# Kernel optimization log

Hardware: AMD Instinct MI355X
Metric: run time of the kernel (lower is better)

## Reference

```python
import jax, jax.numpy as jnp
import numpy as np

T = 0.12  # softmax temperature


def _mlp(x, Wa, ba, Wb, bb, Wc, bc):
    # Linear -> ReLU -> (Dropout=id in eval) -> Linear -> ReLU -> Linear -> ReLU
    h = jax.nn.relu(x @ Wa + ba)
    h = jax.nn.relu(h @ Wb + bb)
    return jax.nn.relu(h @ Wc + bc)


def setup_inputs() -> dict:
    key = jax.random.key(0)
    ks = jax.random.split(key, 16)
    B, K, A, P = 2048, 64, 312, 128
    std = 0.01  # torch init: normal(0, 0.01), bias 0
    inp = {
        "v2s": jax.random.normal(ks[0], (B, A), jnp.float32),
        "tar_atts": jax.random.uniform(ks[1], (B, 1), jnp.float32),
        "sample_indices": jax.random.randint(ks[2], (B, K), 0, B),
        # CLproject[1]: 1 -> 1024 -> 2048 -> 312
        "W2a": std * jax.random.normal(ks[3], (1, 1024), jnp.float32),
        "b2a": jnp.zeros((1024,), jnp.float32),
        "W2b": std * jax.random.normal(ks[4], (1024, 2048), jnp.float32),
        "b2b": jnp.zeros((2048,), jnp.float32),
        "W2c": std * jax.random.normal(ks[5], (2048, A), jnp.float32),
        "b2c": jnp.zeros((A,), jnp.float32),
        # CLproject[0]: 312 -> 1024 -> 2048 -> 128
        "W1a": std * jax.random.normal(ks[6], (A, 1024), jnp.float32),
        "b1a": jnp.zeros((1024,), jnp.float32),
        "W1b": std * jax.random.normal(ks[7], (1024, 2048), jnp.float32),
        "b1b": jnp.zeros((2048,), jnp.float32),
        "W1c": std * jax.random.normal(ks[8], (2048, P), jnp.float32),
        "b1c": jnp.zeros((P,), jnp.float32),
    }
    return inp


def reference(v2s, tar_atts, sample_indices, W2a, b2a, W2b, b2b, W2c, b2c,
              W1a, b1a, W1b, b1b, W1c, b1c):
    # attribute embedding via CLproject[1]: [B,1] -> [B,312]
    att = _mlp(tar_atts, W2a, b2a, W2b, b2b, W2c, b2c)
    v2s_sg = jax.lax.stop_gradient(v2s)  # detach().clone()
    # gather padded pos+neg sample lists: [B,K,312]
    samples = v2s_sg[sample_indices]
    # per-sample projection via CLproject[0]
    proj_samples = _mlp(samples + att[:, None, :], W1a, b1a, W1b, b1b, W1c, b1c)  # [B,K,128]
    query = _mlp(v2s_sg + att, W1a, b1a, W1b, b1b, W1c, b1c)  # [B,128]
    # batched version of per-sample einsum('c,kc->k')
    logits = jnp.einsum("bc,bkc->bk", query, proj_samples) / T
    return logits
```

## Files before the change

### kernel.cpp

```cpp
#include <hip/hip_runtime.h>
#include <stdio.h>
#include <stdint.h>

typedef __attribute__((ext_vector_type(8))) short short8;
typedef __attribute__((ext_vector_type(4))) float f32x4;
typedef __attribute__((ext_vector_type(4))) unsigned short ushort4v;

__device__ __forceinline__ unsigned short f2bf(float f) {
  unsigned int u = __builtin_bit_cast(unsigned int, f);
  u = u + 0x7FFFu + ((u >> 16) & 1u);
  return (unsigned short)(u >> 16);
}
__device__ __forceinline__ float bf2f(unsigned short h) {
  unsigned int u = ((unsigned int)h) << 16;
  return __builtin_bit_cast(float, u);
}

__device__ __forceinline__ void gl_lds16(const unsigned short* g, unsigned short* l) {
  __builtin_amdgcn_global_load_lds(
      (const __attribute__((address_space(1))) unsigned int*)(const void*)g,
      (__attribute__((address_space(3))) unsigned int*)(void*)l, 16, 0, 0);
}

__device__ __forceinline__ int lds_off(int row, int g) {
  int slot = (g + (row >> 1)) & 3;
  return row * 32 + slot * 8;
}

__global__ void k_transpose_cast(const float* __restrict__ in, unsigned short* __restrict__ out,
                                 int Nin, int Kin, int ldo) {
  int k = blockIdx.x * blockDim.x + threadIdx.x;
  int n = blockIdx.y;
  if (k >= ldo) return;
  float v = (n < Nin && k < Kin) ? in[(size_t)k * Nin + n] : 0.f;
  out[(size_t)n * ldo + k] = f2bf(v);
}

__global__ void k_att_l1(const float* __restrict__ tar, const float* __restrict__ W2a,
                         const float* __restrict__ b2a, unsigned short* __restrict__ out) {
  int id = blockIdx.x * 256 + threadIdx.x;
  int b = id >> 10, j = id & 1023;
  out[id] = f2bf(fmaxf(tar[b] * W2a[j] + b2a[j], 0.f));
}

__global__ void k_v2s_cast(const float* __restrict__ v2s, unsigned short* __restrict__ out) {
  int id = blockIdx.x * 256 + threadIdx.x;
  int r = id / 320, c = id - r * 320;
  out[id] = (c < 312) ? f2bf(v2s[(size_t)r * 312 + c]) : (unsigned short)0;
}

__global__ __launch_bounds__(512, 2)
void k_gemm256(const unsigned short* __restrict__ A, const unsigned short* __restrict__ B,
               const float* __restrict__ bias, int nNt, int K,
               unsigned short* __restrict__ outp, int ldo) {
  __shared__ __align__(16) unsigned short sm[3 * 16384];
  int d = blockIdx.x, nwg = gridDim.x;
  int q = nwg >> 3;
  int L = (d & 7) * q + (d >> 3);
  int mt = L / nNt, nt = L - mt * nNt;
  size_t m0 = (size_t)mt * 256, n0 = (size_t)nt * 256;
  int tid = threadIdx.x, lane = tid & 63;
  int w = tid >> 6, wr = w >> 2, wc = w & 3;
  int r0 = tid >> 2;
  int gch = ((tid & 3) - (tid >> 3)) & 3;
  const unsigned short* Asrc0 = A + (m0 + r0) * K + gch * 8;
  const unsigned short* Asrc1 = A + (m0 + r0 + 128) * K + gch * 8;
  const unsigned short* Bsrc0 = B + (n0 + r0) * K + gch * 8;
  const unsigned short* Bsrc1 = B + (n0 + r0 + 128) * K + gch * 8;
  int ldst0 = w * 512;
  int ldst1 = 4096 + w * 512;

#define STAGE(t_, b_) do {                                              \
    int k0_ = (t_) * 32;                                                \
    unsigned short* Ab_ = &sm[(b_) * 16384];                            \
    unsigned short* Bb_ = &sm[(b_) * 16384 + 8192];                     \
    gl_lds16(Asrc0 + k0_, Ab_ + ldst0);                                 \
    gl_lds16(Asrc1 + k0_, Ab_ + ldst1);                                 \
    gl_lds16(Bsrc0 + k0_, Bb_ + ldst0);                                 \
    gl_lds16(Bsrc1 + k0_, Bb_ + ldst1);                                 \
  } while (0)

  int kg = lane >> 4, l15 = lane & 15;
  int aoff = lds_off(wr * 128 + l15, kg);
  int boff = lds_off(wc * 64 + l15, kg);

  f32x4 acc[8][4];
  #pragma unroll
  for (int i = 0; i < 8; ++i)
    #pragma unroll
    for (int j = 0; j < 4; ++j) acc[i][j] = (f32x4)(0.f);

  const int NT = K >> 5;
  STAGE(0, 0);
  STAGE(1, 1);
  asm volatile("s_waitcnt vmcnt(4)" ::: "memory");
  __syncthreads();

  for (int t = 0; t < NT; ++t) {
    int cur = t % 3;
    if (t + 2 < NT) STAGE(t + 2, (t + 2) % 3);
    const unsigned short* Ab = &sm[cur * 16384];
    const unsigned short* Bb = &sm[cur * 16384 + 8192];
    short8 af[8], bfv[4];
    #pragma unroll
    for (int mi = 0; mi < 8; ++mi) af[mi] = *(const short8*)&Ab[aoff + mi * 512];
    #pragma unroll
    for (int ni = 0; ni < 4; ++ni) bfv[ni] = *(const short8*)&Bb[boff + ni * 512];
    __builtin_amdgcn_s_setprio(1);
    #pragma unroll
    for (int mi = 0; mi < 8; ++mi)
      #pragma unroll
      for (int ni = 0; ni < 4; ++ni)
        acc[mi][ni] = __builtin_amdgcn_mfma_f32_16x16x32_bf16(af[mi], bfv[ni], acc[mi][ni], 0, 0, 0);
    __builtin_amdgcn_s_setprio(0);
    if (t + 1 < NT) {
      if (t + 2 < NT) asm volatile("s_waitcnt vmcnt(4)" ::: "memory");
      else            asm volatile("s_waitcnt vmcnt(0)" ::: "memory");
      __syncthreads();
    }
  }
#undef STAGE

  #pragma unroll
  for (int ni = 0; ni < 4; ++ni) {
    int colg = (int)n0 + wc * 64 + ni * 16 + l15;
    float bs = bias[colg];
    #pragma unroll
    for (int mi = 0; mi < 8; ++mi) {
      #pragma unroll
      for (int r2 = 0; r2 < 4; ++r2) {
        size_t rowg = m0 + wr * 128 + mi * 16 + kg * 4 + r2;
        outp[rowg * ldo + colg] = f2bf(fmaxf(acc[mi][ni][r2] + bs, 0.f));
      }
    }
  }
}

template<bool RELU, bool OUTBF16>
__global__ __launch_bounds__(256)
void k_gemm_bt(const unsigned short* __restrict__ A, const unsigned short* __restrict__ B,
               const float* __restrict__ bias, int bias_n, int nNt, int N_store, int K,
               void* __restrict__ outp, int ldo, int remap) {
  __shared__ __align__(16) unsigned short As[128 * 32];
  __shared__ __align__(16) unsigned short Bs[128 * 32];
  int d = blockIdx.x, nwg = gridDim.x;
  int L = d;
  if (remap) { int q = nwg >> 3; L = (d & 7) * q + (d >> 3); }
  int mt = L / nNt, nt = L - mt * nNt;
  size_t m0 = (size_t)mt * 128, n0 = (size_t)nt * 128;
  int tid = threadIdx.x, lane = tid & 63;
  int w = tid >> 6, wr = w >> 1, wc = w & 1;
  int sr = tid >> 2;
  int gch = ((tid & 3) - (tid >> 3)) & 3;
  const unsigned short* pA0 = A + (m0 + sr) * K + gch * 8;
  const unsigned short* pA1 = pA0 + (size_t)64 * K;
  const unsigned short* pB0 = B + (n0 + sr) * K + gch * 8;
  const unsigned short* pB1 = pB0 + (size_t)64 * K;
  unsigned short* lA0 = &As[(tid & ~63) * 8];
  unsigned short* lA1 = &As[64 * 32 + (tid & ~63) * 8];
  unsigned short* lB0 = &Bs[(tid & ~63) * 8];
  unsigned short* lB1 = &Bs[64 * 32 + (tid & ~63) * 8];

  int kg = lane >> 4, l15 = lane & 15;
  int aoff = lds_off(wr * 64 + l15, kg);
  int boff = lds_off(wc * 64 + l15, kg);

  f32x4 acc[4][4];
  #pragma unroll
  for (int i = 0; i < 4; ++i)
    #pragma unroll
    for (int j = 0; j < 4; ++j) acc[i][j] = (f32x4)(0.f);

  for (int k0 = 0; k0 < K; k0 += 32) {
    __syncthreads();
    gl_lds16(pA0 + k0, lA0);
    gl_lds16(pA1 + k0, lA1);
    gl_lds16(pB0 + k0, lB0);
    gl_lds16(pB1 + k0, lB1);
    __syncthreads();
    short8 af[4], bfr[4];
    #pragma unroll
    for (int mi = 0; mi < 4; ++mi) af[mi] = *(const short8*)&As[aoff + mi * 512];
    #pragma unroll
    for (int ni = 0; ni < 4; ++ni) bfr[ni] = *(const short8*)&Bs[boff + ni * 512];
    #pragma unroll
    for (int mi = 0; mi < 4; ++mi)
      #pragma unroll
      for (int ni = 0; ni < 4; ++ni)
        acc[mi][ni] = __builtin_amdgcn_mfma_f32_16x16x32_bf16(af[mi], bfr[ni], acc[mi][ni], 0, 0, 0);
  }

  #pragma unroll
  for (int ni = 0; ni < 4; ++ni) {
    int colg = (int)n0 + wc * 64 + ni * 16 + l15;
    if (colg < N_store) {
      float bs = bias ? (colg < bias_n ? bias[colg] : 0.f) : 0.f;
      #pragma unroll
      for (int mi = 0; mi < 4; ++mi) {
        #pragma unroll
        for (int r2 = 0; r2 < 4; ++r2) {
          size_t rowg = m0 + wr * 64 + mi * 16 + kg * 4 + r2;
          float v = acc[mi][ni][r2] + bs;
          if (RELU) v = fmaxf(v, 0.f);
          if (OUTBF16) ((unsigned short*)outp)[rowg * ldo + colg] = f2bf(v);
          else         ((float*)outp)[rowg * ldo + colg] = v;
        }
      }
    }
  }
}

__global__ void k_build_h1(const float* __restrict__ V1, const float* __restrict__ A1p,
                           const int* __restrict__ idx, unsigned short* __restrict__ H1c,
                           int rbase) {
  int row = rbase + blockIdx.x;
  int src, arow;
  if (row < 2048) { src = row; arow = row; }
  else {
    int g = row - 2048; arow = g >> 6;
    int s = idx[g];
    src = s < 0 ? 0 : (s > 2047 ? 2047 : s);
  }
  int j = threadIdx.x * 4;
  float4 v = *(const float4*)(V1 + (size_t)src * 1024 + j);
  float4 a = *(const float4*)(A1p + (size_t)arow * 1024 + j);
  ushort4v o;
  o.x = f2bf(fmaxf(v.x + a.x, 0.f));
  o.y = f2bf(fmaxf(v.y + a.y, 0.f));
  o.z = f2bf(fmaxf(v.z + a.z, 0.f));
  o.w = f2bf(fmaxf(v.w + a.w, 0.f));
  *(ushort4v*)(H1c + (size_t)blockIdx.x * 1024 + j) = o;
}

__global__ void k_dot(const unsigned short* __restrict__ P, float* __restrict__ out) {
  __shared__ float q[128];
  int b = blockIdx.x, t = threadIdx.x;
  if (t < 128) q[t] = bf2f(P[(size_t)b * 128 + t]);
  __syncthreads();
  int k = t >> 2, part = t & 3;
  const unsigned short* row = P + (size_t)(2048 + b * 64 + k) * 128 + part * 32;
  const float* qp = q + part * 32;
  float s = 0.f;
  #pragma unroll
  for (int j = 0; j < 32; j += 8) {
    short8 pv = *(const short8*)(row + j);
    #pragma unroll
    for (int e = 0; e < 8; ++e)
      s += bf2f((unsigned short)pv[e]) * qp[j + e];
  }
  s += __shfl_xor(s, 1);
  s += __shfl_xor(s, 2);
  if (part == 0) out[(size_t)b * 64 + k] = s * (float)(1.0 / 0.12);
}

extern "C" void kernel_launch(void* const* d_in, const int* in_sizes, int n_in,
                              void* d_out, int out_size, void* d_ws, size_t ws_size,
                              hipStream_t stream) {
  const float* v2s = (const float*)d_in[0];
  const float* tar = (const float*)d_in[1];
  const int*   sidx = (const int*)d_in[2];
  const float* W2a = (const float*)d_in[3];
  const float* b2a = (const float*)d_in[4];
  const float* W2b = (const float*)d_in[5];
  const float* b2b = (const float*)d_in[6];
  const float* W2c = (const float*)d_in[7];
  const float* b2c = (const float*)d_in[8];
  const float* W1a = (const float*)d_in[9];
  const float* b1a = (const float*)d_in[10];
  const float* W1b = (const float*)d_in[11];
  const float* b1b = (const float*)d_in[12];
  const float* W1c = (const float*)d_in[13];
  const float* b1c = (const float*)d_in[14];
  float* out = (float*)d_out;

  char* ws = (char*)d_ws;
  size_t off = 0;
  auto alloc = [&](size_t bytes) -> char* {
    char* p = ws + off; off += (bytes + 255) & ~(size_t)255; return p;
  };
  unsigned short* W1bT = (unsigned short*)alloc(2048ull * 1024 * 2);
  unsigned short* W1cT = (unsigned short*)alloc(128ull * 2048 * 2);
  float*          V1   = (float*)alloc(2048ull * 1024 * 4);
  float*          A1p  = (float*)alloc(2048ull * 1024 * 4);
  unsigned short* Pb   = (unsigned short*)alloc(133120ull * 128 * 2);
  size_t O = off;
  off = O;
  unsigned short* W1aT = (unsigned short*)alloc(1024ull * 320 * 2);
  unsigned short* v2sb = (unsigned short*)alloc(2048ull * 320 * 2);
  unsigned short* attb = (unsigned short*)alloc(2048ull * 320 * 2);
  unsigned short* W2bT = (unsigned short*)alloc(2048ull * 1024 * 2);
  unsigned short* W2cT = (unsigned short*)alloc(384ull * 2048 * 2);
  unsigned short* h_a  = (unsigned short*)alloc(2048ull * 1024 * 2);
  unsigned short* h2a  = (unsigned short*)alloc(2048ull * 2048 * 2);
  size_t early_end = off;

  const int cands[4] = {1, 2, 4, 8};
  int NCH = -1, R = 0;
  for (int ci = 0; ci < 4; ++ci) {
    int c = cands[ci];
    size_t Rr = 133120ull / c;
    size_t late = O + (((Rr * 1024 * 2) + 255) & ~(size_t)255)
                    + (((Rr * 2048 * 2) + 255) & ~(size_t)255);
    size_t need = late > early_end ? late : early_end;
    if (need <= ws_size) { NCH = c; R = (int)Rr; break; }
  }
  int use256 = (NCH > 0);
  if (NCH < 0) {
    size_t Rr = 133120ull / 16;
    size_t late = O + (((Rr * 1024 * 2) + 255) & ~(size_t)255)
                    + (((Rr * 2048 * 2) + 255) & ~(size_t)255);
    size_t need = late > early_end ? late : early_end;
    if (need <= ws_size) { NCH = 16; R = (int)Rr; }
  }
  fprintf(stderr, "[kernel_launch] ws_size=%zu NCH=%d use256=%d\n", ws_size, NCH, use256);
  if (NCH < 0) {
    hipMemsetAsync(d_out, 0, (size_t)out_size * 4, stream);
    return;
  }
  off = O;
  unsigned short* H1c = (unsigned short*)alloc((size_t)R * 1024 * 2);
  unsigned short* H2c = (unsigned short*)alloc((size_t)R * 2048 * 2);

  dim3 blk(256);
  k_transpose_cast<<<dim3(4, 2048), blk, 0, stream>>>(W2b, W2bT, 2048, 1024, 1024);
  k_transpose_cast<<<dim3(8, 384),  blk, 0, stream>>>(W2c, W2cT, 312, 2048, 2048);
  k_transpose_cast<<<dim3(2, 1024), blk, 0, stream>>>(W1a, W1aT, 1024, 312, 320);
  k_transpose_cast<<<dim3(4, 2048), blk, 0, stream>>>(W1b, W1bT, 2048, 1024, 1024);
  k_transpose_cast<<<dim3(8, 128),  blk, 0, stream>>>(W1c, W1cT, 128, 2048, 2048);
  k_att_l1<<<8192, blk, 0, stream>>>(tar, W2a, b2a, h_a);
  k_v2s_cast<<<2560, blk, 0, stream>>>(v2s, v2sb);
  k_gemm_bt<true,  true ><<<256, blk, 0, stream>>>(h_a,  W2bT, b2b, 2048, 16, 2048, 1024, h2a,  2048, 1);
  k_gemm_bt<true,  true ><<<48,  blk, 0, stream>>>(h2a,  W2cT, b2c, 312,  3,  320,  2048, attb, 320,  1);
  k_gemm_bt<false, false><<<128, blk, 0, stream>>>(v2sb, W1aT, nullptr, 0,  8, 1024, 320, V1,  1024, 1);
  k_gemm_bt<false, false><<<128, blk, 0, stream>>>(attb, W1aT, b1a, 1024,  8, 1024, 320, A1p, 1024, 1);
  for (int c = 0; c < NCH; ++c) {
    int rbase = c * R;
    k_build_h1<<<R, blk, 0, stream>>>(V1, A1p, sidx, H1c, rbase);
    if (use256)
      k_gemm256<<<(R / 256) * 8, dim3(512), 0, stream>>>(H1c, W1bT, b1b, 8, 1024, H2c, 2048);
    else
      k_gemm_bt<true, true><<<(R / 128) * 16, blk, 0, stream>>>(H1c, W1bT, b1b, 2048, 16, 2048, 1024, H2c, 2048, 1);
    k_gemm_bt<true, true><<<(R / 128), blk, 0, stream>>>(H2c, W1cT, b1c, 128, 1, 128, 2048,
                                                          Pb + (size_t)rbase * 128, 128, 0);
  }
  k_dot<<<2048, blk, 0, stream>>>(Pb, out);
}
```

Before: 1.166 ms.

## Restructure 256x256 GEMM into 8-wave ping-pong schedule with 64-wide K tiles

```diff
diff --git a/kernel.cpp b/kernel.cpp
--- a/kernel.cpp
+++ b/kernel.cpp
@@ -22,10 +22,9 @@
       (__attribute__((address_space(3))) unsigned int*)(void*)l, 16, 0, 0);
 }
 
-__device__ __forceinline__ int lds_off(int row, int g) {
-  int slot = (g + (row >> 1)) & 3;
-  return row * 32 + slot * 8;
-}
+#define RAW_BAR()  asm volatile("s_barrier" ::: "memory")
+#define LGKM0()    asm volatile("s_waitcnt lgkmcnt(0)" ::: "memory")
+#define VMCNT(n_)  asm volatile("s_waitcnt vmcnt(" #n_ ")" ::: "memory")
 
 __global__ void k_transpose_cast(const float* __restrict__ in, unsigned short* __restrict__ out,
                                  int Nin, int Kin, int ldo) {
@@ -50,39 +49,38 @@
 }
 
 __global__ __launch_bounds__(512, 2)
-void k_gemm256(const unsigned short* __restrict__ A, const unsigned short* __restrict__ B,
-               const float* __restrict__ bias, int nNt, int K,
-               unsigned short* __restrict__ outp, int ldo) {
-  __shared__ __align__(16) unsigned short sm[3 * 16384];
-  int d = blockIdx.x, nwg = gridDim.x;
+void k_gemm256p8(const unsigned short* __restrict__ A, const unsigned short* __restrict__ B,
+                 const float* __restrict__ bias, int nNt, int K,
+                 unsigned short* __restrict__ outp, int ldo) {
+  __shared__ __align__(16) unsigned short sm[65536];
+  int d0 = blockIdx.x, nwg = gridDim.x;
   int q = nwg >> 3;
-  int L = (d & 7) * q + (d >> 3);
+  int L = (d0 & 7) * q + (d0 >> 3);
   int mt = L / nNt, nt = L - mt * nNt;
   size_t m0 = (size_t)mt * 256, n0 = (size_t)nt * 256;
   int tid = threadIdx.x, lane = tid & 63;
   int w = tid >> 6, wr = w >> 2, wc = w & 3;
-  int r0 = tid >> 2;
-  int gch = ((tid & 3) - (tid >> 3)) & 3;
-  const unsigned short* Asrc0 = A + (m0 + r0) * K + gch * 8;
-  const unsigned short* Asrc1 = A + (m0 + r0 + 128) * K + gch * 8;
-  const unsigned short* Bsrc0 = B + (n0 + r0) * K + gch * 8;
-  const unsigned short* Bsrc1 = B + (n0 + r0 + 128) * K + gch * 8;
-  int ldst0 = w * 512;
-  int ldst1 = 4096 + w * 512;
-
-#define STAGE(t_, b_) do {                                              \
-    int k0_ = (t_) * 32;                                                \
-    unsigned short* Ab_ = &sm[(b_) * 16384];                            \
-    unsigned short* Bb_ = &sm[(b_) * 16384 + 8192];                     \
-    gl_lds16(Asrc0 + k0_, Ab_ + ldst0);                                 \
-    gl_lds16(Asrc1 + k0_, Ab_ + ldst1);                                 \
-    gl_lds16(Bsrc0 + k0_, Bb_ + ldst0);                                 \
-    gl_lds16(Bsrc1 + k0_, Bb_ + ldst1);                                 \
+
+  int srow = tid >> 3;
+  int gch = ((tid & 7) - srow) & 7;
+  const unsigned short* Asrc = A + (m0 + srow) * K + gch * 8;
+  const unsigned short* Bsrc = B + (n0 + srow) * K + gch * 8;
+  int sdst = w * 512;
+
+#define STAGE_A(u_, h_) do { int db_ = ((u_) & 1) * 32768, ko_ = (u_) * 64;          \
+    gl_lds16(Asrc + ((h_) * 128 + 0 ) * K + ko_, sm + db_ + (h_) * 8192 + 0    + sdst); \
+    gl_lds16(Asrc + ((h_) * 128 + 64) * K + ko_, sm + db_ + (h_) * 8192 + 4096 + sdst); \
   } while (0)
+#define STAGE_B(u_, h_) do { int db_ = ((u_) & 1) * 32768 + 16384, ko_ = (u_) * 64;  \
+    gl_lds16(Bsrc + ((h_) * 128 + 0 ) * K + ko_, sm + db_ + (h_) * 8192 + 0    + sdst); \
+    gl_lds16(Bsrc + ((h_) * 128 + 64) * K + ko_, sm + db_ + (h_) * 8192 + 4096 + sdst); \
+  } while (0)
 
   int kg = lane >> 4, l15 = lane & 15;
-  int aoff = lds_off(wr * 128 + l15, kg);
-  int boff = lds_off(wc * 64 + l15, kg);
+  int CA = wr * 128 + l15;
+  int CB = wc * 64 + l15;
+  int aoffs[2] = { CA * 64 + ((kg + CA) & 7) * 8, CA * 64 + ((kg + CA + 4) & 7) * 8 };
+  int boffs[2] = { CB * 64 + ((kg + CB) & 7) * 8, CB * 64 + ((kg + CB + 4) & 7) * 8 };
 
   f32x4 acc[8][4];
   #pragma unroll
@@ -90,36 +88,87 @@
     #pragma unroll
     for (int j = 0; j < 4; ++j) acc[i][j] = (f32x4)(0.f);
 
-  const int NT = K >> 5;
-  STAGE(0, 0);
-  STAGE(1, 1);
-  asm volatile("s_waitcnt vmcnt(4)" ::: "memory");
-  __syncthreads();
-
-  for (int t = 0; t < NT; ++t) {
-    int cur = t % 3;
-    if (t + 2 < NT) STAGE(t + 2, (t + 2) % 3);
-    const unsigned short* Ab = &sm[cur * 16384];
-    const unsigned short* Bb = &sm[cur * 16384 + 8192];
-    short8 af[8], bfv[4];
-    #pragma unroll
-    for (int mi = 0; mi < 8; ++mi) af[mi] = *(const short8*)&Ab[aoff + mi * 512];
-    #pragma unroll
-    for (int ni = 0; ni < 4; ++ni) bfv[ni] = *(const short8*)&Bb[boff + ni * 512];
+  const int NT = K >> 6;
+
+  STAGE_A(0, 0); STAGE_A(0, 1); STAGE_B(0, 0); STAGE_B(0, 1);
+  STAGE_B(1, 0); STAGE_B(1, 1);
+  VMCNT(4);
+  RAW_BAR();
+
+  short8 af[4][2], bfv[4][2];
+  for (int u = 0; u < NT; ++u) {
+    const unsigned short* Ab = sm + (u & 1) * 32768;
+    const unsigned short* Bb = Ab + 16384;
+    #pragma unroll
+    for (int mi = 0; mi < 4; ++mi)
+      #pragma unroll
+      for (int ks = 0; ks < 2; ++ks) af[mi][ks] = *(const short8*)&Ab[aoffs[ks] + mi * 1024];
+    #pragma unroll
+    for (int ni = 0; ni < 2; ++ni)
+      #pragma unroll
+      for (int ks = 0; ks < 2; ++ks) bfv[ni][ks] = *(const short8*)&Bb[boffs[ks] + ni * 1024];
+    if (u + 1 < NT) STAGE_A(u + 1, 0);
+    RAW_BAR(); LGKM0();
     __builtin_amdgcn_s_setprio(1);
     #pragma unroll
-    for (int mi = 0; mi < 8; ++mi)
-      #pragma unroll
-      for (int ni = 0; ni < 4; ++ni)
-        acc[mi][ni] = __builtin_amdgcn_mfma_f32_16x16x32_bf16(af[mi], bfv[ni], acc[mi][ni], 0, 0, 0);
+    for (int mi = 0; mi < 4; ++mi)
+      #pragma unroll
+      for (int ni = 0; ni < 2; ++ni)
+        #pragma unroll
+        for (int ks = 0; ks < 2; ++ks)
+          acc[mi][ni] = __builtin_amdgcn_mfma_f32_16x16x32_bf16(af[mi][ks], bfv[ni][ks], acc[mi][ni], 0, 0, 0);
     __builtin_amdgcn_s_setprio(0);
-    if (t + 1 < NT) {
-      if (t + 2 < NT) asm volatile("s_waitcnt vmcnt(4)" ::: "memory");
-      else            asm volatile("s_waitcnt vmcnt(0)" ::: "memory");
-      __syncthreads();
+    RAW_BAR();
+    #pragma unroll
+    for (int ni = 2; ni < 4; ++ni)
+      #pragma unroll
+      for (int ks = 0; ks < 2; ++ks) bfv[ni][ks] = *(const short8*)&Bb[boffs[ks] + ni * 1024];
+    if (u + 1 < NT) STAGE_A(u + 1, 1);
+    RAW_BAR(); LGKM0();
+    __builtin_amdgcn_s_setprio(1);
+    #pragma unroll
+    for (int mi = 0; mi < 4; ++mi)
+      #pragma unroll
+      for (int ni = 2; ni < 4; ++ni)
+        #pragma unroll
+        for (int ks = 0; ks < 2; ++ks)
+          acc[mi][ni] = __builtin_amdgcn_mfma_f32_16x16x32_bf16(af[mi][ks], bfv[ni][ks], acc[mi][ni], 0, 0, 0);
+    __builtin_amdgcn_s_setprio(0);
+    RAW_BAR();
+    #pragma unroll
+    for (int mi = 0; mi < 4; ++mi)
+      #pragma unroll
+      for (int ks = 0; ks < 2; ++ks) af[mi][ks] = *(const short8*)&Ab[aoffs[ks] + (mi + 4) * 1024];
+    if (u + 2 < NT) STAGE_B(u + 2, 0);
+    RAW_BAR(); LGKM0();
+    __builtin_amdgcn_s_setprio(1);
+    #pragma unroll
+    for (int mi = 0; mi < 4; ++mi)
+      #pragma unroll
+      for (int ni = 0; ni < 2; ++ni)
+        #pragma unroll
+        for (int ks = 0; ks < 2; ++ks)
+          acc[mi + 4][ni] = __builtin_amdgcn_mfma_f32_16x16x32_bf16(af[mi][ks], bfv[ni][ks], acc[mi + 4][ni], 0, 0, 0);
+    __builtin_amdgcn_s_setprio(0);
+    RAW_BAR();
+    if (u + 2 < NT) STAGE_B(u + 2, 1);
+    __builtin_amdgcn_s_setprio(1);
+    #pragma unroll
+    for (int mi = 0; mi < 4; ++mi)
+      #pragma unroll
+      for (int ni = 2; ni < 4; ++ni)
+        #pragma unroll
+        for (int ks = 0; ks < 2; ++ks)
+          acc[mi + 4][ni] = __builtin_amdgcn_mfma_f32_16x16x32_bf16(af[mi][ks], bfv[ni][ks], acc[mi + 4][ni], 0, 0, 0);
+    __builtin_amdgcn_s_setprio(0);
+    if (u + 1 < NT) {
+      if (u + 2 < NT) { VMCNT(4); }
+      else            { VMCNT(0); }
+      RAW_BAR();
     }
   }
-#undef STAGE
+#undef STAGE_A
+#undef STAGE_B
 
   #pragma unroll
   for (int ni = 0; ni < 4; ++ni) {
@@ -134,6 +183,11 @@
       }
     }
   }
+}
+
+__device__ __forceinline__ int lds_off(int row, int g) {
+  int slot = (g + (row >> 1)) & 3;
+  return row * 32 + slot * 8;
 }
 
 template<bool RELU, bool OUTBF16>
@@ -337,7 +391,7 @@
     int rbase = c * R;
     k_build_h1<<<R, blk, 0, stream>>>(V1, A1p, sidx, H1c, rbase);
     if (use256)
-      k_gemm256<<<(R / 256) * 8, dim3(512), 0, stream>>>(H1c, W1bT, b1b, 8, 1024, H2c, 2048);
+      k_gemm256p8<<<(R / 256) * 8, dim3(512), 0, stream>>>(H1c, W1bT, b1b, 8, 1024, H2c, 2048);
     else
       k_gemm_bt<true, true><<<(R / 128) * 16, blk, 0, stream>>>(H1c, W1bT, b1b, 2048, 16, 2048, 1024, H2c, 2048, 1);
     k_gemm_bt<true, true><<<(R / 128), blk, 0, stream>>>(H2c, W1cT, b1c, 128, 1, 128, 2048,
```

After: 1.143 ms. No clear change (-2.0%).
